# Kernel tuning notes

Hardware: AMD Instinct MI355X
Metric: run time of the kernel (lower is better)

Reference implementation:

```python
import jax, jax.numpy as jnp
import numpy as np

HIGH, LOW = 768, 384
LOW2 = LOW // 2  # PNL uses low_dim // reduc_ratio, reduc_ratio=2
B, N = 8, 4096
EPS = 1e-5


def _nl_block(x_h, x_l, wg, bg, wt, bt, wp, bp, ww, bw, gamma, beta):
    # x_h: [B,N,H], x_l: [B,N0,H]; conv1x1 == per-token linear
    Nl = x_l.shape[1]
    g = jnp.einsum('bnc,dc->bnd', x_l, wg) + bg      # [B,N0,D]
    th = jnp.einsum('bnc,dc->bnd', x_h, wt) + bt     # [B,N,D]
    ph = jnp.einsum('bnc,dc->bnd', x_l, wp) + bp     # [B,N0,D]
    # attention = (th @ ph^T) / N0; y = attention @ g. Reassociate:
    kv = jnp.einsum('bnd,bne->bde', ph, g) / Nl      # [B,D,D]
    y = jnp.einsum('bnd,bde->bne', th, kv)           # [B,N,D]
    y = jnp.einsum('bnd,cd->bnc', y, ww) + bw        # [B,N,H]
    # BatchNorm1d over channel dim, training-mode batch stats (biased var)
    mu = y.mean(axis=(0, 1))
    var = y.var(axis=(0, 1))
    y = (y - mu) * jax.lax.rsqrt(var + EPS) * gamma + beta
    return y + x_h


def setup_inputs() -> dict:
    key = jax.random.key(0)
    ks = jax.random.split(key, 24)
    s = 0.02
    d = {
        'x': jax.random.normal(ks[0], (B, N, HIGH), jnp.float32),
        'x0': jax.random.normal(ks[1], (B, N, HIGH), jnp.float32),
        # CNL params (low_dim = 384)
        'c_wg': s * jax.random.normal(ks[2], (LOW, HIGH)), 'c_bg': s * jax.random.normal(ks[3], (LOW,)),
        'c_wt': s * jax.random.normal(ks[4], (LOW, HIGH)), 'c_bt': s * jax.random.normal(ks[5], (LOW,)),
        'c_wp': s * jax.random.normal(ks[6], (LOW, HIGH)), 'c_bp': s * jax.random.normal(ks[7], (LOW,)),
        'c_ww': s * jax.random.normal(ks[8], (HIGH, LOW)), 'c_bw': s * jax.random.normal(ks[9], (HIGH,)),
        'c_gamma': 1.0 + 0.1 * jax.random.normal(ks[10], (HIGH,)),
        'c_beta': s * jax.random.normal(ks[11], (HIGH,)),
        # PNL params (low_dim // 2 = 192)
        'p_wg': s * jax.random.normal(ks[12], (LOW2, HIGH)), 'p_bg': s * jax.random.normal(ks[13], (LOW2,)),
        'p_wt': s * jax.random.normal(ks[14], (LOW2, HIGH)), 'p_bt': s * jax.random.normal(ks[15], (LOW2,)),
        'p_wp': s * jax.random.normal(ks[16], (LOW2, HIGH)), 'p_bp': s * jax.random.normal(ks[17], (LOW2,)),
        'p_ww': s * jax.random.normal(ks[18], (HIGH, LOW2)), 'p_bw': s * jax.random.normal(ks[19], (HIGH,)),
        'p_gamma': 1.0 + 0.1 * jax.random.normal(ks[20], (HIGH,)),
        'p_beta': s * jax.random.normal(ks[21], (HIGH,)),
    }
    return d


def reference(x, x0,
              c_wg, c_bg, c_wt, c_bt, c_wp, c_bp, c_ww, c_bw, c_gamma, c_beta,
              p_wg, p_bg, p_wt, p_bt, p_wp, p_bp, p_ww, p_bw, p_gamma, p_beta):
    z = _nl_block(x, x0, c_wg, c_bg, c_wt, c_bt, c_wp, c_bp, c_ww, c_bw, c_gamma, c_beta)
    out = _nl_block(z, x0, p_wg, p_bg, p_wt, p_bt, p_wp, p_bp, p_ww, p_bw, p_gamma, p_beta)
    return out
```

## Files before the change

kernel.cpp:

```cpp
#include <hip/hip_runtime.h>
#include <stdint.h>

typedef unsigned short u16;
typedef __bf16 bf16x8 __attribute__((ext_vector_type(8)));
typedef short s16x8 __attribute__((ext_vector_type(8)));
typedef short s16x4 __attribute__((ext_vector_type(4)));
typedef float f32x4 __attribute__((ext_vector_type(4)));

__device__ __forceinline__ u16 f2bf(float f) {
  uint32_t u = __builtin_bit_cast(uint32_t, f);
  u += 0x7fffu + ((u >> 16) & 1u);
  return (u16)(u >> 16);
}
__device__ __forceinline__ float bf2f(u16 h) {
  uint32_t u = ((uint32_t)h) << 16;
  return __builtin_bit_cast(float, u);
}

__device__ __forceinline__ void gl16(const u16* g, u16* l) {
  __builtin_amdgcn_global_load_lds(
      (const __attribute__((address_space(1))) void*)g,
      (__attribute__((address_space(3))) void*)l, 16, 0, 0);
}

__device__ __forceinline__ void barf() {
  asm volatile("s_barrier" ::: "memory");
}

__device__ __forceinline__ int src_chunk(int l) {
  return (((l & 3) ^ ((l >> 3) & 3)) * 8);
}
__device__ __forceinline__ int rd_koff(int l) {
  return (((l >> 4) ^ (((l & 15) >> 1) & 3)) * 8);
}

__global__ void cvt_in2(const float* __restrict__ a, const float* __restrict__ b,
                        u16* __restrict__ da, u16* __restrict__ db, long n8each) {
  long stride = (long)gridDim.x * blockDim.x;
  long total = 2 * n8each;
  for (long i = (long)blockIdx.x * blockDim.x + threadIdx.x; i < total; i += stride) {
    const float* src = (i < n8each) ? a + i * 8 : b + (i - n8each) * 8;
    u16* dst = (i < n8each) ? da + i * 8 : db + (i - n8each) * 8;
    const f32x4* s = (const f32x4*)src;
    f32x4 v0 = s[0], v1 = s[1];
    s16x8 o;
#pragma unroll
    for (int j = 0; j < 4; ++j) o[j] = (short)f2bf(v0[j]);
#pragma unroll
    for (int j = 0; j < 4; ++j) o[4 + j] = (short)f2bf(v1[j]);
    *(s16x8*)dst = o;
  }
}

__global__ void cvt_flat8(const float* __restrict__ src, u16* __restrict__ dst,
                          long n8, float scale) {
  long stride = (long)gridDim.x * blockDim.x;
  for (long i = (long)blockIdx.x * blockDim.x + threadIdx.x; i < n8; i += stride) {
    const f32x4* s = (const f32x4*)(src + i * 8);
    f32x4 a = s[0], b = s[1];
    s16x8 o;
#pragma unroll
    for (int j = 0; j < 4; ++j) o[j] = (short)f2bf(a[j] * scale);
#pragma unroll
    for (int j = 0; j < 4; ++j) o[4 + j] = (short)f2bf(b[j] * scale);
    *(s16x8*)(dst + i * 8) = o;
  }
}

__global__ void prep_w(const float* __restrict__ c_wg, const float* __restrict__ c_wp,
                       const float* __restrict__ p_wg, const float* __restrict__ p_wp,
                       const float* __restrict__ c_wt, const float* __restrict__ p_wt,
                       const float* __restrict__ c_ww, const float* __restrict__ p_ww,
                       u16* __restrict__ wcat, u16* __restrict__ wt_c,
                       u16* __restrict__ wt_p, u16* __restrict__ ww_c,
                       u16* __restrict__ ww_p) {
  const int C0 = 1280 * 768 / 4;
  const int C1 = C0 + 384 * 768 / 4;
  const int C2 = C1 + 256 * 768 / 4;
  const int C3 = C2 + 768 * 384 / 4;
  const int C4 = C3 + 768 * 256 / 4;
  int stride = gridDim.x * blockDim.x;
  for (int i = blockIdx.x * blockDim.x + threadIdx.x; i < C4; i += stride) {
    const float* src = nullptr;
    u16* dst;
    if (i < C0) {
      int e = i * 4;
      dst = wcat + e;
      int r = e / 768;
      if (r < 384) src = c_wg + e;
      else if (r < 768) src = c_wp + e - 384 * 768;
      else if (r < 960) src = p_wg + e - 768 * 768;
      else if (r < 1024) src = nullptr;
      else if (r < 1216) src = p_wp + e - 1024 * 768;
      else src = nullptr;
    } else if (i < C1) {
      int e = (i - C0) * 4; dst = wt_c + e; src = c_wt + e;
    } else if (i < C2) {
      int e = (i - C1) * 4; dst = wt_p + e;
      src = (e / 768 < 192) ? p_wt + e : nullptr;
    } else if (i < C3) {
      int e = (i - C2) * 4; dst = ww_c + e; src = c_ww + e;
    } else {
      int e = (i - C3) * 4; dst = ww_p + e;
      int r = e >> 8, c = e & 255;
      src = (c < 192) ? p_ww + r * 192 + c : nullptr;
    }
    s16x4 o;
    if (src) {
      f32x4 v = *(const f32x4*)src;
#pragma unroll
      for (int j = 0; j < 4; ++j) o[j] = (short)f2bf(v[j]);
    } else {
      o = s16x4{0, 0, 0, 0};
    }
    *(s16x4*)dst = o;
  }
}

__global__ void prep_b(const float* __restrict__ c_bg, const float* __restrict__ c_bp,
                       const float* __restrict__ p_bg, const float* __restrict__ p_bp,
                       const float* __restrict__ c_bt, const float* __restrict__ p_bt,
                       float* __restrict__ biasb, float* __restrict__ sums) {
  int i = blockIdx.x * blockDim.x + threadIdx.x;
  if (i < 1920) {
    float v = 0.f;
    if (i < 384) v = c_bg[i];
    else if (i < 768) v = c_bp[i - 384];
    else if (i < 960) v = p_bg[i - 768];
    else if (i < 1024) v = 0.f;
    else if (i < 1216) v = p_bp[i - 1024];
    else if (i < 1280) v = 0.f;
    else if (i < 1664) v = c_bt[i - 1280];
    else if (i < 1856) v = p_bt[i - 1664];
    biasb[i] = v;
  } else if (i < 1920 + 24576) {
    sums[i - 1920] = 0.f;
  }
}

template <int BIAS, int SUMS>
__global__ __launch_bounds__(512) void gemm_nt_big(
    const u16* __restrict__ A, const u16* __restrict__ B, void* __restrict__ Cv,
    const float* __restrict__ bias, float* __restrict__ sums,
    int ntiles, long lda, long ldb, long ldc, int K,
    long aBatch, long bBatch, long cBatch) {
  __shared__ u16 As[4][256 * 32];
  __shared__ u16 Bs[4][256 * 32];

  const int bm = blockIdx.x / ntiles;
  const int bn = blockIdx.x % ntiles;
  const int bb = blockIdx.y;
  const int nt = K >> 5;

  const u16* Ab = A + (long)bb * aBatch + (long)bm * 256 * lda;
  const u16* Bb = B + (long)bb * bBatch + (long)bn * 256 * ldb;

  const int t = threadIdx.x;
  const int w = t >> 6;
  const int l = t & 63;
  const int wr = w >> 2;
  const int wc = w & 3;

  const int srow = w * 16 + (l >> 2);
  const int cg = src_chunk(l);
  const long aoff0 = (long)srow * lda + cg;
  const long aoff1 = (long)(128 + srow) * lda + cg;
  const long boff0 = (long)srow * ldb + cg;
  const long boff1 = (long)(128 + srow) * ldb + cg;

#define STAGE_A(T, BUF)                                   \
  gl16(Ab + aoff0 + (long)(T) * 32, &As[BUF][w * 512]);   \
  gl16(Ab + aoff1 + (long)(T) * 32, &As[BUF][(8 + w) * 512]);
#define STAGE_B(T, BUF)                                   \
  gl16(Bb + boff0 + (long)(T) * 32, &Bs[BUF][w * 512]);   \
  gl16(Bb + boff1 + (long)(T) * 32, &Bs[BUF][(8 + w) * 512]);

  f32x4 acc[8][4] = {};

  STAGE_A(0, 0); STAGE_B(0, 0);
  if (nt > 1) { STAGE_A(1, 1); STAGE_B(1, 1); }
  if (nt > 2) { STAGE_A(2, 2); STAGE_B(2, 2); }

  const int koff = rd_koff(l);
  const int ar = wr * 128 + (l & 15);
  const int br = wc * 64 + (l & 15);

  for (int tt = 0; tt < nt; ++tt) {
    const int cur = tt & 3;
    const int ahead = nt - 1 - tt;
    if (ahead >= 2)      asm volatile("s_waitcnt vmcnt(8)" ::: "memory");
    else if (ahead == 1) asm volatile("s_waitcnt vmcnt(4)" ::: "memory");
    else                 asm volatile("s_waitcnt vmcnt(0)" ::: "memory");
    barf();

    if (tt + 3 < nt) {
      const int pf = (tt + 3) & 3;
      STAGE_A(tt + 3, pf);
      STAGE_B(tt + 3, pf);
    }

    bf16x8 bfr[4], af[8];
#pragma unroll
    for (int ni = 0; ni < 4; ++ni)
      bfr[ni] = __builtin_bit_cast(
          bf16x8, *(const s16x8*)(&Bs[cur][(br + ni * 16) * 32 + koff]));
#pragma unroll
    for (int mi = 0; mi < 8; ++mi)
      af[mi] = __builtin_bit_cast(
          bf16x8, *(const s16x8*)(&As[cur][(ar + mi * 16) * 32 + koff]));
    __builtin_amdgcn_s_setprio(1);
#pragma unroll
    for (int mi = 0; mi < 8; ++mi)
#pragma unroll
      for (int ni = 0; ni < 4; ++ni)
        acc[mi][ni] = __builtin_amdgcn_mfma_f32_16x16x32_bf16(
            af[mi], bfr[ni], acc[mi][ni], 0, 0, 0);
    __builtin_amdgcn_s_setprio(0);
  }
#undef STAGE_A
#undef STAGE_B
  __builtin_amdgcn_sched_barrier(0);

  const long crow0 = (long)bm * 256 + wr * 128;
  const long ccol0 = (long)bn * 256 + wc * 64;
  u16* C = (u16*)Cv + (long)bb * cBatch;
#pragma unroll
  for (int mi = 0; mi < 8; ++mi)
#pragma unroll
    for (int j = 0; j < 4; ++j) {
      long row = crow0 + mi * 16 + (l >> 4) * 4 + j;
      float rb = (BIAS == 1) ? bias[row] : 0.f;
#pragma unroll
      for (int ni = 0; ni < 4; ++ni) {
        long col = ccol0 + ni * 16 + (l & 15);
        C[row * ldc + col] = f2bf(acc[mi][ni][j] + rb);
      }
    }

  if (SUMS) {
    float* srep = sums + (blockIdx.x & 7) * 1536;
#pragma unroll
    for (int ni = 0; ni < 4; ++ni) {
      float s = 0.f, q = 0.f;
#pragma unroll
      for (int mi = 0; mi < 8; ++mi)
#pragma unroll
        for (int j = 0; j < 4; ++j) {
          float v = acc[mi][ni][j];
          s += v;
          q += v * v;
        }
      s += __shfl_xor(s, 16);
      q += __shfl_xor(q, 16);
      s += __shfl_xor(s, 32);
      q += __shfl_xor(q, 32);
      if (l < 16) {
        long col = ccol0 + ni * 16 + l;
        atomicAdd(&srep[col], s);
        atomicAdd(&srep[768 + col], q);
      }
    }
  }
}

template <int BIAS, int OUT_ATOMIC, int SUMS>
__global__ __launch_bounds__(256) void gemm_nt(
    const u16* __restrict__ A, const u16* __restrict__ B, void* __restrict__ Cv,
    const float* __restrict__ bias, float* __restrict__ sums,
    int ntiles, long lda, long ldb, long ldc, int K,
    long aBatch, long bBatch, long cBatch) {
  __shared__ u16 As[3][128 * 32];
  __shared__ u16 Bs[3][128 * 32];

  const int bm = blockIdx.x / ntiles;
  const int bn = blockIdx.x % ntiles;
  const int bb = blockIdx.y;
  const int kChunk = K / gridDim.z;
  const long k0base = (long)blockIdx.z * kChunk;
  const int nt = kChunk >> 5;

  const u16* Ab = A + (long)bb * aBatch + (long)bm * 128 * lda + k0base;
  const u16* Bb = B + (long)bb * bBatch + (long)bn * 128 * ldb + k0base;

  const int t = threadIdx.x;
  const int w = t >> 6;
  const int l = t & 63;
  const int wr = w >> 1, wc = w & 1;

  const int cg = src_chunk(l);
  const long aoff = (long)(32 * w + (l >> 2)) * lda + cg;
  const long boff = (long)(32 * w + (l >> 2)) * ldb + cg;

  f32x4 acc[4][4] = {};

#define STG(T, BUF)                                          \
  gl16(Ab + aoff + (long)(T) * 32, &As[BUF][(32 * w) * 32]); \
  gl16(Ab + aoff + 16 * lda + (long)(T) * 32, &As[BUF][(32 * w + 16) * 32]); \
  gl16(Bb + boff + (long)(T) * 32, &Bs[BUF][(32 * w) * 32]); \
  gl16(Bb + boff + 16 * ldb + (long)(T) * 32, &Bs[BUF][(32 * w + 16) * 32]);

  STG(0, 0);
  if (nt > 1) { STG(1, 1); }

  const int koff = rd_koff(l);

  for (int tt = 0; tt < nt; ++tt) {
    const int cur = tt % 3;
    if (tt + 1 < nt)
      asm volatile("s_waitcnt vmcnt(4)" ::: "memory");
    else
      asm volatile("s_waitcnt vmcnt(0)" ::: "memory");
    barf();

    if (tt + 2 < nt) {
      const int pf = (tt + 2) % 3;
      STG(tt + 2, pf);
    }

    bf16x8 af[4], bfr[4];
#pragma unroll
    for (int mi = 0; mi < 4; ++mi)
      af[mi] = __builtin_bit_cast(
          bf16x8, *(const s16x8*)(&As[cur][(wr * 64 + mi * 16 + (l & 15)) * 32 + koff]));
#pragma unroll
    for (int ni = 0; ni < 4; ++ni)
      bfr[ni] = __builtin_bit_cast(
          bf16x8, *(const s16x8*)(&Bs[cur][(wc * 64 + ni * 16 + (l & 15)) * 32 + koff]));
    __builtin_amdgcn_s_setprio(1);
#pragma unroll
    for (int mi = 0; mi < 4; ++mi)
#pragma unroll
      for (int ni = 0; ni < 4; ++ni)
        acc[mi][ni] = __builtin_amdgcn_mfma_f32_16x16x32_bf16(
            af[mi], bfr[ni], acc[mi][ni], 0, 0, 0);
    __builtin_amdgcn_s_setprio(0);
  }
#undef STG
  __builtin_amdgcn_sched_barrier(0);

  const long crow0 = (long)bm * 128 + wr * 64;
  const long ccol0 = (long)bn * 128 + wc * 64;

  if (OUT_ATOMIC) {
    float* C = (float*)Cv + (long)bb * cBatch;
#pragma unroll
    for (int mi = 0; mi < 4; ++mi)
#pragma unroll
      for (int j = 0; j < 4; ++j) {
        long row = crow0 + mi * 16 + (l >> 4) * 4 + j;
#pragma unroll
        for (int ni = 0; ni < 4; ++ni) {
          long col = ccol0 + ni * 16 + (l & 15);
          atomicAdd(&C[row * ldc + col], acc[mi][ni][j]);
        }
      }
  } else {
    u16* C = (u16*)Cv + (long)bb * cBatch;
#pragma unroll
    for (int mi = 0; mi < 4; ++mi)
#pragma unroll
      for (int j = 0; j < 4; ++j) {
        long row = crow0 + mi * 16 + (l >> 4) * 4 + j;
        float rb = (BIAS == 1) ? bias[row] : 0.f;
#pragma unroll
        for (int ni = 0; ni < 4; ++ni) {
          long col = ccol0 + ni * 16 + (l & 15);
          float cb = (BIAS == 2) ? bias[col] : 0.f;
          C[row * ldc + col] = f2bf(acc[mi][ni][j] + rb + cb);
        }
      }
  }

  if (SUMS) {
    float* srep = sums + (blockIdx.x & 7) * 1536;
#pragma unroll
    for (int ni = 0; ni < 4; ++ni) {
      float s = 0.f, q = 0.f;
#pragma unroll
      for (int mi = 0; mi < 4; ++mi)
#pragma unroll
        for (int j = 0; j < 4; ++j) {
          float v = acc[mi][ni][j];
          s += v;
          q += v * v;
        }
      s += __shfl_xor(s, 16);
      q += __shfl_xor(q, 16);
      s += __shfl_xor(s, 32);
      q += __shfl_xor(q, 32);
      if (l < 16) {
        long col = ccol0 + ni * 16 + l;
        atomicAdd(&srep[col], s);
        atomicAdd(&srep[768 + col], q);
      }
    }
  }
}

__global__ void bn_stats(const float* __restrict__ sums, const float* __restrict__ gamma,
                         const float* __restrict__ beta, float* __restrict__ stats,
                         float invN) {
  int c = threadIdx.x;
  float s = 0.f, q = 0.f;
#pragma unroll
  for (int r = 0; r < 8; ++r) {
    s += sums[r * 1536 + c];
    q += sums[r * 1536 + 768 + c];
  }
  float mu = s * invN;
  float var = q * invN - mu * mu;
  float sc = gamma[c] * rsqrtf(var + 1e-5f);
  stats[c] = sc;
  stats[768 + c] = beta[c] - mu * sc;
}

template <int OUT_F32>
__global__ void bn_apply(const u16* __restrict__ pre, const u16* __restrict__ resid,
                         const float* __restrict__ stats, void* __restrict__ out,
                         long n8) {
  long stride = (long)gridDim.x * blockDim.x;
  for (long i = (long)blockIdx.x * blockDim.x + threadIdx.x; i < n8; i += stride) {
    long base = i * 8;
    int c = (int)(base % 768);
    f32x4 sc0 = *(const f32x4*)(stats + c);
    f32x4 sc1 = *(const f32x4*)(stats + c + 4);
    f32x4 sh0 = *(const f32x4*)(stats + 768 + c);
    f32x4 sh1 = *(const f32x4*)(stats + 768 + c + 4);
    s16x8 p = *(const s16x8*)(pre + base);
    s16x8 rv = *(const s16x8*)(resid + base);
    float o[8];
#pragma unroll
    for (int j = 0; j < 4; ++j)
      o[j] = bf2f((u16)p[j]) * sc0[j] + sh0[j] + bf2f((u16)rv[j]);
#pragma unroll
    for (int j = 0; j < 4; ++j)
      o[4 + j] = bf2f((u16)p[4 + j]) * sc1[j] + sh1[j] + bf2f((u16)rv[4 + j]);
    if (OUT_F32) {
      f32x4 o0, o1;
#pragma unroll
      for (int j = 0; j < 4; ++j) { o0[j] = o[j]; o1[j] = o[4 + j]; }
      f32x4* op = (f32x4*)((float*)out + base);
      op[0] = o0;
      op[1] = o1;
    } else {
      s16x8 ov;
#pragma unroll
      for (int j = 0; j < 8; ++j) ov[j] = (short)f2bf(o[j]);
      *(s16x8*)((u16*)out + base) = ov;
    }
  }
}

extern "C" void kernel_launch(void* const* d_in, const int* in_sizes, int n_in,
                              void* d_out, int out_size, void* d_ws, size_t ws_size,
                              hipStream_t stream) {
  const float* x = (const float*)d_in[0];
  const float* x0 = (const float*)d_in[1];
  const float* c_wg = (const float*)d_in[2];
  const float* c_bg = (const float*)d_in[3];
  const float* c_wt = (const float*)d_in[4];
  const float* c_bt = (const float*)d_in[5];
  const float* c_wp = (const float*)d_in[6];
  const float* c_bp = (const float*)d_in[7];
  const float* c_ww = (const float*)d_in[8];
  const float* c_gamma = (const float*)d_in[10];
  const float* c_beta = (const float*)d_in[11];
  const float* p_wg = (const float*)d_in[12];
  const float* p_bg = (const float*)d_in[13];
  const float* p_wt = (const float*)d_in[14];
  const float* p_bt = (const float*)d_in[15];
  const float* p_wp = (const float*)d_in[16];
  const float* p_bp = (const float*)d_in[17];
  const float* p_ww = (const float*)d_in[18];
  const float* p_gamma = (const float*)d_in[20];
  const float* p_beta = (const float*)d_in[21];

  char* ws = (char*)d_ws;
  const long NT = 32768;
  u16* xbf = (u16*)(ws + 0);
  u16* x0bf = (u16*)(ws + 50331648);
  u16* th = (u16*)(ws + 50331648);
  float* kvf_c = (float*)(ws + 75497472);
  float* kvf_p = (float*)(ws + 80216064);
  u16* kvb = (u16*)(ws + 82313216);
  u16* kvwT = (u16*)(ws + 84672512);
  u16* gphT = (u16*)(ws + 100663296);
  u16* wcat = (u16*)(ws + 184549376);
  u16* wt_c = (u16*)(ws + 186515456);
  u16* wt_p = (u16*)(ws + 187105280);
  u16* ww_c = (u16*)(ws + 187498496);
  u16* ww_p = (u16*)(ws + 188088320);
  float* biasb = (float*)(ws + 188481536);
  float* sums = (float*)(ws + 188489216);
  float* stats = (float*)(ws + 188587520);
  u16* zbf = xbf;
  u16* pre = gphT;

  cvt_in2<<<4096, 256, 0, stream>>>(x, x0, xbf, x0bf, NT * 768 / 8);
  prep_w<<<480, 256, 0, stream>>>(c_wg, c_wp, p_wg, p_wp, c_wt, p_wt, c_ww, p_ww,
                                  wcat, wt_c, wt_p, ww_c, ww_p);
  prep_b<<<104, 256, 0, stream>>>(c_bg, c_bp, p_bg, p_bp, c_bt, p_bt, biasb, sums);

  gemm_nt_big<1, 0><<<dim3(5 * 128, 1, 1), 512, 0, stream>>>(
      wcat, x0bf, gphT, biasb, nullptr, 128, 768, 768, 32768, 768, 0, 0, 0);
  hipMemsetAsync(kvf_c, 0, 4718592 + 2097152, stream);

  gemm_nt<2, 0, 0><<<dim3(256 * 3, 1, 1), 256, 0, stream>>>(
      xbf, wt_c, th, biasb + 1280, nullptr, 3, 768, 768, 384, 768, 0, 0, 0);
  gemm_nt<0, 1, 0><<<dim3(9, 8, 8), 256, 0, stream>>>(
      gphT + (long)384 * 32768, gphT, kvf_c, nullptr, nullptr, 3, 32768, 32768,
      384, 4096, 4096, 4096, (long)384 * 384);
  cvt_flat8<<<576, 256, 0, stream>>>(kvf_c, kvb, (long)8 * 384 * 384 / 8, 1.f / 4096.f);
  gemm_nt<0, 0, 0><<<dim3(18, 8, 1), 256, 0, stream>>>(
      ww_c, kvb, kvwT, nullptr, nullptr, 3, 384, 384, 384, 384, 0,
      (long)384 * 384, (long)768 * 384);
  gemm_nt_big<0, 1><<<dim3(48, 8, 1), 512, 0, stream>>>(
      th, kvwT, pre, nullptr, sums, 3, 384, 384, 768, 384, (long)4096 * 384,
      (long)768 * 384, (long)4096 * 768);
  bn_stats<<<1, 768, 0, stream>>>(sums, c_gamma, c_beta, stats, 1.f / 32768.f);
  bn_apply<0><<<2048, 256, 0, stream>>>(pre, xbf, stats, zbf, NT * 768 / 8);

  gemm_nt<2, 0, 0><<<dim3(256 * 2, 1, 1), 256, 0, stream>>>(
      zbf, wt_p, th, biasb + 1664, nullptr, 2, 768, 768, 256, 768, 0, 0, 0);
  gemm_nt<0, 1, 0><<<dim3(4, 8, 8), 256, 0, stream>>>(
      gphT + (long)1024 * 32768, gphT + (long)768 * 32768, kvf_p, nullptr, nullptr,
      2, 32768, 32768, 256, 4096, 4096, 4096, (long)256 * 256);
  cvt_flat8<<<256, 256, 0, stream>>>(kvf_p, kvb, (long)8 * 256 * 256 / 8, 1.f / 4096.f);
  gemm_nt<0, 0, 0><<<dim3(12, 8, 1), 256, 0, stream>>>(
      ww_p, kvb, kvwT, nullptr, nullptr, 2, 256, 256, 256, 256, 0,
      (long)256 * 256, (long)768 * 256);
  gemm_nt_big<0, 1><<<dim3(48, 8, 1), 512, 0, stream>>>(
      th, kvwT, pre, nullptr, sums + 8 * 1536, 3, 256, 256, 768, 256,
      (long)4096 * 256, (long)768 * 256, (long)4096 * 768);
  bn_stats<<<1, 768, 0, stream>>>(sums + 8 * 1536, p_gamma, p_beta, stats, 1.f / 32768.f);
  bn_apply<1><<<2048, 256, 0, stream>>>(pre, zbf, stats, (float*)d_out, NT * 768 / 8);
}
```

Before: 470.9 us.

## Restructure GEMM LDS pipelines: two-tile steps in big kernel, double-buffer in small

The 256x256 GEMM now prefetches four K-tiles up front and processes two tiles per loop iteration. It waits once per pair and refills both freed buffers after a second barrier, which halves the vmcnt waits and barriers per K-tile. The 128x128 GEMM drops from triple to double buffering, reissuing loads into the just-consumed buffer after a post-compute barrier, and removes the setprio hints. This cuts LDS use and may raise occupancy, but the loads now have less time to land before they are needed. The big kernel assumes nt is even and at least 4 with no guard.

```diff
diff --git a/kernel.cpp b/kernel.cpp
--- a/kernel.cpp
+++ b/kernel.cpp
@@ -178,44 +178,66 @@
   f32x4 acc[8][4] = {};
 
   STAGE_A(0, 0); STAGE_B(0, 0);
-  if (nt > 1) { STAGE_A(1, 1); STAGE_B(1, 1); }
-  if (nt > 2) { STAGE_A(2, 2); STAGE_B(2, 2); }
+  STAGE_A(1, 1); STAGE_B(1, 1);
+  STAGE_A(2, 2); STAGE_B(2, 2);
+  STAGE_A(3, 3); STAGE_B(3, 3);
 
   const int koff = rd_koff(l);
   const int ar = wr * 128 + (l & 15);
   const int br = wc * 64 + (l & 15);
 
-  for (int tt = 0; tt < nt; ++tt) {
-    const int cur = tt & 3;
-    const int ahead = nt - 1 - tt;
-    if (ahead >= 2)      asm volatile("s_waitcnt vmcnt(8)" ::: "memory");
-    else if (ahead == 1) asm volatile("s_waitcnt vmcnt(4)" ::: "memory");
-    else                 asm volatile("s_waitcnt vmcnt(0)" ::: "memory");
+  for (int tt = 0; tt < nt; tt += 2) {
+    if (tt + 4 <= nt) asm volatile("s_waitcnt vmcnt(8)" ::: "memory");
+    else              asm volatile("s_waitcnt vmcnt(0)" ::: "memory");
     barf();
 
-    if (tt + 3 < nt) {
-      const int pf = (tt + 3) & 3;
-      STAGE_A(tt + 3, pf);
-      STAGE_B(tt + 3, pf);
-    }
-
-    bf16x8 bfr[4], af[8];
-#pragma unroll
-    for (int ni = 0; ni < 4; ++ni)
-      bfr[ni] = __builtin_bit_cast(
-          bf16x8, *(const s16x8*)(&Bs[cur][(br + ni * 16) * 32 + koff]));
-#pragma unroll
-    for (int mi = 0; mi < 8; ++mi)
-      af[mi] = __builtin_bit_cast(
-          bf16x8, *(const s16x8*)(&As[cur][(ar + mi * 16) * 32 + koff]));
-    __builtin_amdgcn_s_setprio(1);
-#pragma unroll
-    for (int mi = 0; mi < 8; ++mi)
+    const int c0 = tt & 3;
+    const int c1 = (tt + 1) & 3;
+
+    {
+      bf16x8 bfr[4], af[8];
 #pragma unroll
       for (int ni = 0; ni < 4; ++ni)
-        acc[mi][ni] = __builtin_amdgcn_mfma_f32_16x16x32_bf16(
-            af[mi], bfr[ni], acc[mi][ni], 0, 0, 0);
-    __builtin_amdgcn_s_setprio(0);
+        bfr[ni] = __builtin_bit_cast(
+            bf16x8, *(const s16x8*)(&Bs[c0][(br + ni * 16) * 32 + koff]));
+#pragma unroll
+      for (int mi = 0; mi < 8; ++mi)
+        af[mi] = __builtin_bit_cast(
+            bf16x8, *(const s16x8*)(&As[c0][(ar + mi * 16) * 32 + koff]));
+      __builtin_amdgcn_s_setprio(1);
+#pragma unroll
+      for (int mi = 0; mi < 8; ++mi)
+#pragma unroll
+        for (int ni = 0; ni < 4; ++ni)
+          acc[mi][ni] = __builtin_amdgcn_mfma_f32_16x16x32_bf16(
+              af[mi], bfr[ni], acc[mi][ni], 0, 0, 0);
+      __builtin_amdgcn_s_setprio(0);
+    }
+    {
+      bf16x8 bfr[4], af[8];
+#pragma unroll
+      for (int ni = 0; ni < 4; ++ni)
+        bfr[ni] = __builtin_bit_cast(
+            bf16x8, *(const s16x8*)(&Bs[c1][(br + ni * 16) * 32 + koff]));
+#pragma unroll
+      for (int mi = 0; mi < 8; ++mi)
+        af[mi] = __builtin_bit_cast(
+            bf16x8, *(const s16x8*)(&As[c1][(ar + mi * 16) * 32 + koff]));
+      __builtin_amdgcn_s_setprio(1);
+#pragma unroll
+      for (int mi = 0; mi < 8; ++mi)
+#pragma unroll
+        for (int ni = 0; ni < 4; ++ni)
+          acc[mi][ni] = __builtin_amdgcn_mfma_f32_16x16x32_bf16(
+              af[mi], bfr[ni], acc[mi][ni], 0, 0, 0);
+      __builtin_amdgcn_s_setprio(0);
+    }
+
+    barf();
+    if (tt + 4 < nt) {
+      STAGE_A(tt + 4, c0); STAGE_B(tt + 4, c0);
+      STAGE_A(tt + 5, c1); STAGE_B(tt + 5, c1);
+    }
   }
 #undef STAGE_A
 #undef STAGE_B
@@ -269,8 +291,8 @@
     const float* __restrict__ bias, float* __restrict__ sums,
     int ntiles, long lda, long ldb, long ldc, int K,
     long aBatch, long bBatch, long cBatch) {
-  __shared__ u16 As[3][128 * 32];
-  __shared__ u16 Bs[3][128 * 32];
+  __shared__ u16 As[2][128 * 32];
+  __shared__ u16 Bs[2][128 * 32];
 
   const int bm = blockIdx.x / ntiles;
   const int bn = blockIdx.x % ntiles;
@@ -293,29 +315,26 @@
 
   f32x4 acc[4][4] = {};
 
-#define STG(T, BUF)                                          \
-  gl16(Ab + aoff + (long)(T) * 32, &As[BUF][(32 * w) * 32]); \
-  gl16(Ab + aoff + 16 * lda + (long)(T) * 32, &As[BUF][(32 * w + 16) * 32]); \
-  gl16(Bb + boff + (long)(T) * 32, &Bs[BUF][(32 * w) * 32]); \
-  gl16(Bb + boff + 16 * ldb + (long)(T) * 32, &Bs[BUF][(32 * w + 16) * 32]);
-
-  STG(0, 0);
-  if (nt > 1) { STG(1, 1); }
+  gl16(Ab + aoff, &As[0][(32 * w) * 32]);
+  gl16(Ab + aoff + 16 * lda, &As[0][(32 * w + 16) * 32]);
+  gl16(Bb + boff, &Bs[0][(32 * w) * 32]);
+  gl16(Bb + boff + 16 * ldb, &Bs[0][(32 * w + 16) * 32]);
+  if (nt > 1) {
+    gl16(Ab + aoff + 32, &As[1][(32 * w) * 32]);
+    gl16(Ab + aoff + 16 * lda + 32, &As[1][(32 * w + 16) * 32]);
+    gl16(Bb + boff + 32, &Bs[1][(32 * w) * 32]);
+    gl16(Bb + boff + 16 * ldb + 32, &Bs[1][(32 * w + 16) * 32]);
+  }
 
   const int koff = rd_koff(l);
 
   for (int tt = 0; tt < nt; ++tt) {
-    const int cur = tt % 3;
+    const int cur = tt & 1;
     if (tt + 1 < nt)
       asm volatile("s_waitcnt vmcnt(4)" ::: "memory");
     else
       asm volatile("s_waitcnt vmcnt(0)" ::: "memory");
-    barf();
-
-    if (tt + 2 < nt) {
-      const int pf = (tt + 2) % 3;
-      STG(tt + 2, pf);
-    }
+    __builtin_amdgcn_s_barrier();
 
     bf16x8 af[4], bfr[4];
 #pragma unroll
@@ -326,16 +345,22 @@
     for (int ni = 0; ni < 4; ++ni)
       bfr[ni] = __builtin_bit_cast(
           bf16x8, *(const s16x8*)(&Bs[cur][(wc * 64 + ni * 16 + (l & 15)) * 32 + koff]));
-    __builtin_amdgcn_s_setprio(1);
 #pragma unroll
     for (int mi = 0; mi < 4; ++mi)
 #pragma unroll
       for (int ni = 0; ni < 4; ++ni)
         acc[mi][ni] = __builtin_amdgcn_mfma_f32_16x16x32_bf16(
             af[mi], bfr[ni], acc[mi][ni], 0, 0, 0);
-    __builtin_amdgcn_s_setprio(0);
-  }
-#undef STG
+
+    __builtin_amdgcn_s_barrier();
+    if (tt + 2 < nt) {
+      const long ko = (long)(tt + 2) * 32;
+      gl16(Ab + aoff + ko, &As[cur][(32 * w) * 32]);
+      gl16(Ab + aoff + 16 * lda + ko, &As[cur][(32 * w + 16) * 32]);
+      gl16(Bb + boff + ko, &Bs[cur][(32 * w) * 32]);
+      gl16(Bb + boff + 16 * ldb + ko, &Bs[cur][(32 * w + 16) * 32]);
+    }
+  }
   __builtin_amdgcn_sched_barrier(0);
 
   const long crow0 = (long)bm * 128 + wr * 64;
@@ -371,7 +396,7 @@
       }
   }
 
-  if (SUMS) {
+  if (SUMS && !OUT_ATOMIC) {
     float* srep = sums + (blockIdx.x & 7) * 1536;
 #pragma unroll
     for (int ni = 0; ni < 4; ++ni) {
```

Measured after the change: 455.7 us. -3.2%, faster.
